# Kernel optimization log

Hardware: AMD Instinct MI355X
Metric: run time of the kernel (lower is better)

## Reference

```python
import jax, jax.numpy as jnp
import numpy as np

D_MODEL = 1024
N_HEADS = 16
HEAD_DIM = D_MODEL // N_HEADS
D_FF = 4096
EPS = 1e-5


def setup_inputs() -> dict:
    key = jax.random.key(0)
    ks = jax.random.split(key, 12)
    s = 0.02
    return {
        "x": jax.random.normal(ks[0], (2, 2048, D_MODEL), jnp.float32),
        "wq": jax.random.normal(ks[1], (D_MODEL, D_MODEL), jnp.float32) * s,
        "bq": jnp.zeros((D_MODEL,), jnp.float32),
        "wk": jax.random.normal(ks[2], (D_MODEL, D_MODEL), jnp.float32) * s,
        "bk": jnp.zeros((D_MODEL,), jnp.float32),
        "wv": jax.random.normal(ks[3], (D_MODEL, D_MODEL), jnp.float32) * s,
        "bv": jnp.zeros((D_MODEL,), jnp.float32),
        "wo": jax.random.normal(ks[4], (D_MODEL, D_MODEL), jnp.float32) * s,
        "bo": jnp.zeros((D_MODEL,), jnp.float32),
        "w1": jax.random.normal(ks[5], (D_MODEL, D_FF), jnp.float32) * s,
        "b1": jnp.zeros((D_FF,), jnp.float32),
        "w2": jax.random.normal(ks[6], (D_FF, D_MODEL), jnp.float32) * s,
        "b2": jnp.zeros((D_MODEL,), jnp.float32),
        "g1": jnp.ones((D_MODEL,), jnp.float32),
        "be1": jnp.zeros((D_MODEL,), jnp.float32),
        "g2": jnp.ones((D_MODEL,), jnp.float32),
        "be2": jnp.zeros((D_MODEL,), jnp.float32),
    }


def _layer_norm(x, g, b):
    mu = jnp.mean(x, axis=-1, keepdims=True)
    var = jnp.var(x, axis=-1, keepdims=True)
    return (x - mu) * jax.lax.rsqrt(var + EPS) * g + b


def reference(x, wq, bq, wk, bk, wv, bv, wo, bo, w1, b1, w2, b2, g1, be1, g2, be2):
    B, S, D = x.shape
    nx = _layer_norm(x, g1, be1)
    # projections -> [B, H, S, d]
    def split_heads(t):
        return t.reshape(B, S, N_HEADS, HEAD_DIM).transpose(0, 2, 1, 3)
    q = split_heads(nx @ wq + bq)
    k = split_heads(nx @ wk + bk)
    v = split_heads(nx @ wv + bv)
    scores = jnp.einsum("bhqd,bhkd->bhqk", q, k) / jnp.sqrt(jnp.float32(HEAD_DIM))
    attn = jax.nn.softmax(scores, axis=-1)
    out = jnp.einsum("bhqk,bhkd->bhqd", attn, v)
    out = out.transpose(0, 2, 1, 3).reshape(B, S, D)
    x = x + (out @ wo + bo)
    nx = _layer_norm(x, g2, be2)
    ff = jax.nn.relu(nx @ w1 + b1) @ w2 + b2
    return x + ff
```

## Files before the change

kernel.cpp:

```cpp
#include <hip/hip_runtime.h>


typedef __attribute__((ext_vector_type(8))) unsigned short u16x8;
typedef __attribute__((ext_vector_type(4))) unsigned short u16x4;
typedef __attribute__((ext_vector_type(8))) __bf16 bf16x8;
typedef __attribute__((ext_vector_type(4))) float f32x4;
typedef __attribute__((ext_vector_type(4))) unsigned int u32x4;

#define C_SCALE 0.1803368801111f

static __device__ __forceinline__ unsigned short f2b(float f) {
    return __builtin_bit_cast(unsigned short, (__bf16)f);
}
static __device__ __forceinline__ float b2f(unsigned short h) {
    unsigned u = ((unsigned)h) << 16;
    float f;
    __builtin_memcpy(&f, &u, 4);
    return f;
}

static __device__ __forceinline__ void async_cp16(
    const unsigned short* g, unsigned short* l)
{
    __builtin_amdgcn_global_load_lds(
        (const __attribute__((address_space(1))) unsigned int*)g,
        (__attribute__((address_space(3))) unsigned int*)l,
        16, 0, 0);
}

__global__ __launch_bounds__(256) void transpose_all_k(
    const float* __restrict__ wq, const float* __restrict__ wk,
    const float* __restrict__ wv, const float* __restrict__ wo,
    const float* __restrict__ w1, const float* __restrict__ w2,
    unsigned short* __restrict__ wqkvT, unsigned short* __restrict__ woT,
    unsigned short* __restrict__ w1T, unsigned short* __restrict__ w2T)
{
    __shared__ unsigned short tile[32][33];
    const int ti = blockIdx.x;
    const float* in;
    unsigned short* out;
    int R, C, bi, bj;
    float sc = 1.0f;
    if (ti < 4096) {
        R = 1024; C = 1024;
        bi = (ti & 1023) >> 5; bj = ti & 31;
        int z = ti >> 10;
        in = (z == 0) ? wq : (z == 1) ? wk : (z == 2) ? wv : wo;
        out = (z < 3) ? wqkvT + (size_t)z * 1024 * 1024 : woT;
        if (z == 1) sc = C_SCALE;
    } else if (ti < 8192) {
        R = 1024; C = 4096;
        int l = ti - 4096;
        bi = l >> 7; bj = l & 127;
        in = w1; out = w1T;
    } else {
        R = 4096; C = 1024;
        int l = ti - 8192;
        bi = l >> 5; bj = l & 31;
        in = w2; out = w2T;
    }
    const int tx = threadIdx.x & 31, ty = threadIdx.x >> 5;
#pragma unroll
    for (int rr = 0; rr < 4; ++rr) {
        int r = ty + rr * 8;
        tile[r][tx] = f2b(in[(size_t)(bi * 32 + r) * C + bj * 32 + tx] * sc);
    }
    __syncthreads();
#pragma unroll
    for (int rr = 0; rr < 4; ++rr) {
        int r = ty + rr * 8;
        out[(size_t)(bj * 32 + r) * R + bi * 32 + tx] = tile[tx][r];
    }
}

__global__ __launch_bounds__(256) void concat3_k(
    const float* __restrict__ a, const float* __restrict__ b,
    const float* __restrict__ c, float* __restrict__ o)
{
    int t = blockIdx.x * 256 + threadIdx.x;
    float v = (t < 1024) ? a[t]
            : ((t < 2048) ? b[t - 1024] * C_SCALE : c[t - 2048]);
    o[t] = v;
}

__global__ __launch_bounds__(256) void ln_kernel(
    const float* __restrict__ x, const float* __restrict__ g,
    const float* __restrict__ be, unsigned short* __restrict__ o)
{
    const int row = blockIdx.x;
    const int t = threadIdx.x;
    const float* xr = x + (size_t)row * 1024;
    float4 v4 = *reinterpret_cast<const float4*>(&xr[t * 4]);
    float f[4] = {v4.x, v4.y, v4.z, v4.w};
    float s = f[0] + f[1] + f[2] + f[3];
    float ss = f[0] * f[0] + f[1] * f[1] + f[2] * f[2] + f[3] * f[3];
#pragma unroll
    for (int d = 1; d < 64; d <<= 1) {
        s += __shfl_xor(s, d);
        ss += __shfl_xor(ss, d);
    }
    __shared__ float sb[4], ssb[4];
    const int wave = t >> 6;
    if ((t & 63) == 0) { sb[wave] = s; ssb[wave] = ss; }
    __syncthreads();
    s = sb[0] + sb[1] + sb[2] + sb[3];
    ss = ssb[0] + ssb[1] + ssb[2] + ssb[3];
    const float mu = s * (1.0f / 1024.0f);
    const float var = ss * (1.0f / 1024.0f) - mu * mu;
    const float rs = rsqrtf(var + 1e-5f);
    u16x4 r4;
#pragma unroll
    for (int j = 0; j < 4; ++j)
        r4[j] = f2b((f[j] - mu) * rs * g[t * 4 + j] + be[t * 4 + j]);
    *reinterpret_cast<u16x4*>(&o[(size_t)row * 1024 + t * 4]) = r4;
}

__global__ __launch_bounds__(256) void reduce_ln_kernel(
    const unsigned short* __restrict__ pa, const unsigned short* __restrict__ pb,
    const float* __restrict__ bias, const float* __restrict__ x,
    const float* __restrict__ g, const float* __restrict__ be,
    float* __restrict__ x2, unsigned short* __restrict__ o)
{
    const int row = blockIdx.x;
    const int t = threadIdx.x;
    const size_t base = (size_t)row * 1024 + t * 4;
    float4 x4 = *reinterpret_cast<const float4*>(&x[base]);
    float4 bb = *reinterpret_cast<const float4*>(&bias[t * 4]);
    float f[4] = {x4.x + bb.x, x4.y + bb.y, x4.z + bb.z, x4.w + bb.w};
#pragma unroll
    for (int z = 0; z < 2; ++z) {
        u16x4 va = *reinterpret_cast<const u16x4*>(&pa[(size_t)z * 4096 * 1024 + base]);
        u16x4 vb = *reinterpret_cast<const u16x4*>(&pb[(size_t)z * 4096 * 1024 + base]);
#pragma unroll
        for (int j = 0; j < 4; ++j) f[j] += b2f(va[j]) + b2f(vb[j]);
    }
    *reinterpret_cast<float4*>(&x2[base]) = {f[0], f[1], f[2], f[3]};
    float s = f[0] + f[1] + f[2] + f[3];
    float ss = f[0] * f[0] + f[1] * f[1] + f[2] * f[2] + f[3] * f[3];
#pragma unroll
    for (int d = 1; d < 64; d <<= 1) {
        s += __shfl_xor(s, d);
        ss += __shfl_xor(ss, d);
    }
    __shared__ float sb[4], ssb[4];
    const int wave = t >> 6;
    if ((t & 63) == 0) { sb[wave] = s; ssb[wave] = ss; }
    __syncthreads();
    s = sb[0] + sb[1] + sb[2] + sb[3];
    ss = ssb[0] + ssb[1] + ssb[2] + ssb[3];
    const float mu = s * (1.0f / 1024.0f);
    const float var = ss * (1.0f / 1024.0f) - mu * mu;
    const float rs = rsqrtf(var + 1e-5f);
    u16x4 r4;
#pragma unroll
    for (int j = 0; j < 4; ++j)
        r4[j] = f2b((f[j] - mu) * rs * g[t * 4 + j] + be[t * 4 + j]);
    *reinterpret_cast<u16x4*>(&o[base]) = r4;
}

__global__ __launch_bounds__(256) void reduce_out4_k(
    const unsigned short* __restrict__ pa, const unsigned short* __restrict__ pb,
    const float* __restrict__ bias, const float* __restrict__ x2,
    float* __restrict__ out)
{
    const size_t i4 = ((size_t)blockIdx.x * 256 + threadIdx.x) * 4;
    float4 x4 = *reinterpret_cast<const float4*>(&x2[i4]);
    float4 bb = *reinterpret_cast<const float4*>(&bias[i4 & 1023]);
    float a0 = x4.x + bb.x, a1 = x4.y + bb.y, a2 = x4.z + bb.z, a3 = x4.w + bb.w;
#pragma unroll
    for (int z = 0; z < 2; ++z) {
        u16x4 va = *reinterpret_cast<const u16x4*>(&pa[(size_t)z * 4096 * 1024 + i4]);
        u16x4 vb = *reinterpret_cast<const u16x4*>(&pb[(size_t)z * 4096 * 1024 + i4]);
        a0 += b2f(va[0]) + b2f(vb[0]);
        a1 += b2f(va[1]) + b2f(vb[1]);
        a2 += b2f(va[2]) + b2f(vb[2]);
        a3 += b2f(va[3]) + b2f(vb[3]);
    }
    *reinterpret_cast<float4*>(&out[i4]) = {a0, a1, a2, a3};
}

template<int MODE, int RELU>
__global__ __launch_bounds__(256, 4) void gemm_bt(
    const unsigned short* __restrict__ A, int lda,
    const unsigned short* __restrict__ Bt, int ldb,
    const float* __restrict__ bias,
    void* __restrict__ Cv, void* __restrict__ Cv2, int N, int Kloop)
{
    __shared__ unsigned short As[128 * 32];
    __shared__ unsigned short Bs[128 * 32];
    const int t = threadIdx.x;
    const int wave = t >> 6, lane = t & 63;
    const int quad = lane >> 4, l16 = lane & 15;
    const int wm = wave >> 1, wn = wave & 1;
    const int m0 = blockIdx.y * 128;
    const int n0 = blockIdx.x * 128;
    const int k0 = blockIdx.z * Kloop;
    const int rl = lane >> 2;
    const int cl = (lane & 3) * 8;

    f32x4 acc[4][4];
#pragma unroll
    for (int mi = 0; mi < 4; ++mi)
#pragma unroll
        for (int ni = 0; ni < 4; ++ni) acc[mi][ni] = {0.f, 0.f, 0.f, 0.f};

    for (int kt = 0; kt < Kloop; kt += 32) {
#pragma unroll
        for (int j = 0; j < 4; ++j) {
            int c = wave * 4 + j;
            if (c < 8) {
                async_cp16(&A[(size_t)(m0 + c * 16 + rl) * lda + k0 + kt + cl],
                           &As[c * 512 + lane * 8]);
            } else {
                int bc = c - 8;
                async_cp16(&Bt[(size_t)(n0 + bc * 16 + rl) * ldb + k0 + kt + cl],
                           &Bs[bc * 512 + lane * 8]);
            }
        }
        __syncthreads();
        bf16x8 af[4], bfr[4];
#pragma unroll
        for (int mi = 0; mi < 4; ++mi)
            af[mi] = __builtin_bit_cast(bf16x8,
                *reinterpret_cast<const u16x8*>(&As[(wm * 64 + mi * 16 + l16) * 32 + quad * 8]));
#pragma unroll
        for (int ni = 0; ni < 4; ++ni)
            bfr[ni] = __builtin_bit_cast(bf16x8,
                *reinterpret_cast<const u16x8*>(&Bs[(wn * 64 + ni * 16 + l16) * 32 + quad * 8]));
#pragma unroll
        for (int mi = 0; mi < 4; ++mi)
#pragma unroll
            for (int ni = 0; ni < 4; ++ni)
                acc[mi][ni] = __builtin_amdgcn_mfma_f32_16x16x32_bf16(
                    af[mi], bfr[ni], acc[mi][ni], 0, 0, 0);
        __syncthreads();
    }

#pragma unroll
    for (int mi = 0; mi < 4; ++mi) {
        const int gr0 = m0 + wm * 64 + mi * 16 + quad * 4;
#pragma unroll
        for (int ni = 0; ni < 4; ++ni) {
            const int gc = n0 + wn * 64 + ni * 16 + l16;
            if (MODE == 2) {
                const float bv = bias[gc];
                if (gc < 2048) {
#pragma unroll
                    for (int r = 0; r < 4; ++r)
                        ((unsigned short*)Cv)[(size_t)(gr0 + r) * 2048 + gc] =
                            f2b(acc[mi][ni][r] + bv);
                } else {
                    u16x4 pk;
#pragma unroll
                    for (int r = 0; r < 4; ++r) pk[r] = f2b(acc[mi][ni][r] + bv);
                    const int b = gr0 >> 11, s0 = gr0 & 2047;
                    *reinterpret_cast<u16x4*>(
                        &((unsigned short*)Cv2)[((size_t)b * 1024 + (gc - 2048)) * 2048 + s0]) = pk;
                }
            } else if (MODE == 5) {
                unsigned short* base = (blockIdx.z < 2)
                    ? (unsigned short*)Cv  + (size_t)blockIdx.z * 4096 * N
                    : (unsigned short*)Cv2 + (size_t)(blockIdx.z - 2) * 4096 * N;
#pragma unroll
                for (int r = 0; r < 4; ++r)
                    base[(size_t)(gr0 + r) * N + gc] = f2b(acc[mi][ni][r]);
            } else {
                const float bv = bias[gc];
#pragma unroll
                for (int r = 0; r < 4; ++r) {
                    float v = acc[mi][ni][r] + bv;
                    if (RELU) v = fmaxf(v, 0.f);
                    ((unsigned short*)Cv)[(size_t)(gr0 + r) * N + gc] = f2b(v);
                }
            }
        }
    }
}

__global__ __launch_bounds__(256, 4) void attn_kernel(
    const unsigned short* __restrict__ qkb, const unsigned short* __restrict__ vbT,
    unsigned short* __restrict__ ao)
{
    __shared__ unsigned short Ks[2][64][72];
    __shared__ unsigned short Vt[2][64][72];
    const int t = threadIdx.x;
    const int lane = t & 63;
    const int quad = lane >> 4, l16 = lane & 15;
    const int wave = t >> 6;
    const int bh = blockIdx.y;
    const int b = bh >> 4, h = bh & 15;
    const int q0 = blockIdx.x * 64 + wave * 16;
    const size_t qk_base = (size_t)b * 2048 * 2048;
    const size_t vt_base = (size_t)b * 1024 * 2048 + (size_t)h * 64 * 2048;

    bf16x8 qf[2];
#pragma unroll
    for (int kk = 0; kk < 2; ++kk)
        qf[kk] = __builtin_bit_cast(bf16x8, *reinterpret_cast<const u16x8*>(
            &qkb[qk_base + (size_t)(q0 + l16) * 2048 + h * 64 + kk * 32 + quad * 8]));

    u16x8 ones_u;
#pragma unroll
    for (int j = 0; j < 8; ++j) ones_u[j] = 0x3F80;
    const bf16x8 onesf = __builtin_bit_cast(bf16x8, ones_u);

    f32x4 o_acc[4], l_frag;
    l_frag = {0.f, 0.f, 0.f, 0.f};
#pragma unroll
    for (int nf = 0; nf < 4; ++nf) o_acc[nf] = {0.f, 0.f, 0.f, 0.f};

    const int srow0 = t >> 3, sc8 = (t & 7) * 8;
    const int srow1 = srow0 + 32;

    const unsigned short* kg0 = &qkb[qk_base + (size_t)srow0 * 2048 + 1024 + h * 64 + sc8];
    const unsigned short* kg1 = kg0 + (size_t)32 * 2048;
    const unsigned short* vg0 = &vbT[vt_base + (size_t)srow0 * 2048 + sc8];
    const unsigned short* vg1 = vg0 + (size_t)32 * 2048;

    u16x8 kr[2], vr[2];
    kr[0] = *reinterpret_cast<const u16x8*>(kg0);
    kr[1] = *reinterpret_cast<const u16x8*>(kg1);
    vr[0] = *reinterpret_cast<const u16x8*>(vg0);
    vr[1] = *reinterpret_cast<const u16x8*>(vg1);
    *reinterpret_cast<u16x8*>(&Ks[0][srow0][sc8]) = kr[0];
    *reinterpret_cast<u16x8*>(&Ks[0][srow1][sc8]) = kr[1];
    *reinterpret_cast<u16x8*>(&Vt[0][srow0][sc8]) = vr[0];
    *reinterpret_cast<u16x8*>(&Vt[0][srow1][sc8]) = vr[1];
    kr[0] = *reinterpret_cast<const u16x8*>(kg0 + (size_t)64 * 2048);
    kr[1] = *reinterpret_cast<const u16x8*>(kg1 + (size_t)64 * 2048);
    vr[0] = *reinterpret_cast<const u16x8*>(vg0 + 64);
    vr[1] = *reinterpret_cast<const u16x8*>(vg1 + 64);
    __syncthreads();

    for (int it = 0; it < 32; ++it) {
        const int cur = it & 1, nxt = cur ^ 1;
        if (it + 1 < 32) {
            *reinterpret_cast<u16x8*>(&Ks[nxt][srow0][sc8]) = kr[0];
            *reinterpret_cast<u16x8*>(&Ks[nxt][srow1][sc8]) = kr[1];
            *reinterpret_cast<u16x8*>(&Vt[nxt][srow0][sc8]) = vr[0];
            *reinterpret_cast<u16x8*>(&Vt[nxt][srow1][sc8]) = vr[1];
        }
        if (it + 2 < 32) {
            const size_t ko = (size_t)(it + 2) * 64 * 2048;
            const int vo = (it + 2) * 64;
            kr[0] = *reinterpret_cast<const u16x8*>(kg0 + ko);
            kr[1] = *reinterpret_cast<const u16x8*>(kg1 + ko);
            vr[0] = *reinterpret_cast<const u16x8*>(vg0 + vo);
            vr[1] = *reinterpret_cast<const u16x8*>(vg1 + vo);
        }

#pragma unroll
        for (int kh = 0; kh < 2; ++kh) {
            unsigned d0[2], d1[2];
#pragma unroll
            for (int kfi = 0; kfi < 2; ++kfi) {
                const int kf = kh * 2 + kfi;
                bf16x8 kfr0 = __builtin_bit_cast(bf16x8,
                    *reinterpret_cast<const u16x8*>(&Ks[cur][kf * 16 + l16][quad * 8]));
                bf16x8 kfr1 = __builtin_bit_cast(bf16x8,
                    *reinterpret_cast<const u16x8*>(&Ks[cur][kf * 16 + l16][32 + quad * 8]));
                f32x4 s = {0.f, 0.f, 0.f, 0.f};
                s = __builtin_amdgcn_mfma_f32_16x16x32_bf16(kfr0, qf[0], s, 0, 0, 0);
                s = __builtin_amdgcn_mfma_f32_16x16x32_bf16(kfr1, qf[1], s, 0, 0, 0);
                d0[kfi] = (unsigned)f2b(exp2f(s[0])) |
                          ((unsigned)f2b(exp2f(s[1])) << 16);
                d1[kfi] = (unsigned)f2b(exp2f(s[2])) |
                          ((unsigned)f2b(exp2f(s[3])) << 16);
            }
            unsigned x0 = d0[0], y0 = d0[1];
            unsigned x1 = d1[0], y1 = d1[1];
            asm("v_permlane32_swap_b32 %0, %1\n\t"
                "v_permlane16_swap_b32 %0, %1"
                : "+v"(x0), "+v"(y0));
            asm("v_permlane32_swap_b32 %0, %1\n\t"
                "v_permlane16_swap_b32 %0, %1"
                : "+v"(x1), "+v"(y1));
            u32x4 pw = {x0, x1, y0, y1};
            bf16x8 pfr = __builtin_bit_cast(bf16x8, pw);
            l_frag = __builtin_amdgcn_mfma_f32_16x16x32_bf16(
                pfr, onesf, l_frag, 0, 0, 0);
            __builtin_amdgcn_s_setprio(1);
#pragma unroll
            for (int nf = 0; nf < 4; ++nf) {
                bf16x8 vfr = __builtin_bit_cast(bf16x8,
                    *reinterpret_cast<const u16x8*>(&Vt[cur][nf * 16 + l16][kh * 32 + quad * 8]));
                o_acc[nf] = __builtin_amdgcn_mfma_f32_16x16x32_bf16(
                    pfr, vfr, o_acc[nf], 0, 0, 0);
            }
            __builtin_amdgcn_s_setprio(0);
        }
        __syncthreads();
    }

#pragma unroll
    for (int r = 0; r < 4; ++r) {
        const float inv = 1.0f / l_frag[r];
        const int row = q0 + quad * 4 + r;
#pragma unroll
        for (int nf = 0; nf < 4; ++nf)
            ao[(size_t)b * 2048 * 1024 + (size_t)row * 1024 + h * 64 + nf * 16 + l16] =
                f2b(o_acc[nf][r] * inv);
    }
}

extern "C" void kernel_launch(void* const* d_in, const int* in_sizes, int n_in,
                              void* d_out, int out_size, void* d_ws, size_t ws_size,
                              hipStream_t stream)
{
    const float* x   = (const float*)d_in[0];
    const float* wq  = (const float*)d_in[1];
    const float* bq  = (const float*)d_in[2];
    const float* wk  = (const float*)d_in[3];
    const float* bk  = (const float*)d_in[4];
    const float* wv  = (const float*)d_in[5];
    const float* bv  = (const float*)d_in[6];
    const float* wo  = (const float*)d_in[7];
    const float* bo  = (const float*)d_in[8];
    const float* w1  = (const float*)d_in[9];
    const float* b1  = (const float*)d_in[10];
    const float* w2  = (const float*)d_in[11];
    const float* b2  = (const float*)d_in[12];
    const float* g1  = (const float*)d_in[13];
    const float* be1 = (const float*)d_in[14];
    const float* g2  = (const float*)d_in[15];
    const float* be2 = (const float*)d_in[16];
    float* out = (float*)d_out;
    char*  ws  = (char*)d_ws;

    const int M = 4096, D = 1024, DFF = 4096;
    const size_t MB = 1 << 20;

    unsigned short* wqkvT = (unsigned short*)(ws + 0 * MB);
    unsigned short* woT   = (unsigned short*)(ws + 6 * MB);
    unsigned short* w1T   = (unsigned short*)(ws + 8 * MB);
    unsigned short* w2T   = (unsigned short*)(ws + 16 * MB);
    unsigned short* ln    = (unsigned short*)(ws + 24 * MB);
    unsigned short* qkb   = (unsigned short*)(ws + 32 * MB);
    unsigned short* vbT   = (unsigned short*)(ws + 48 * MB);
    unsigned short* ao    = (unsigned short*)(ws + 56 * MB);
    unsigned short* ff1   = (unsigned short*)(ws + 32 * MB);
    float*          x2    = (float*)(ws + 64 * MB);
    float*          bqkv  = (float*)(ws + 80 * MB);
    unsigned short* pHi   = (unsigned short*)(ws + 80 * MB);
    unsigned short* pOlo  = (unsigned short*)(ws + 32 * MB);
    unsigned short* pFlo  = (unsigned short*)(ws + 0 * MB);

    transpose_all_k<<<12288, 256, 0, stream>>>(wq, wk, wv, wo, w1, w2,
                                               wqkvT, woT, w1T, w2T);
    concat3_k<<<12, 256, 0, stream>>>(bq, bk, bv, bqkv);
    ln_kernel<<<M, 256, 0, stream>>>(x, g1, be1, ln);
    gemm_bt<2, 0><<<dim3(24, 32), 256, 0, stream>>>(
        ln, D, wqkvT, D, bqkv, qkb, vbT, 3072, D);
    attn_kernel<<<dim3(32, 32), 256, 0, stream>>>(qkb, vbT, ao);
    gemm_bt<5, 0><<<dim3(8, 32, 4), 256, 0, stream>>>(
        ao, D, woT, D, nullptr, pHi, pOlo, 1024, 256);
    reduce_ln_kernel<<<M, 256, 0, stream>>>(pHi, pOlo, bo, x, g2, be2, x2, ln);
    gemm_bt<0, 1><<<dim3(32, 32), 256, 0, stream>>>(
        ln, D, w1T, D, b1, ff1, nullptr, DFF, D);
    gemm_bt<5, 0><<<dim3(8, 32, 4), 256, 0, stream>>>(
        ff1, DFF, w2T, DFF, nullptr, pHi, pFlo, 1024, 1024);
    reduce_out4_k<<<4096, 256, 0, stream>>>(pHi, pFlo, b2, x2, out);
}
```

Before: 378.9 us.

## Add 256x256-tile triple-buffered GEMM kernel for QKV, FF1 and FF2

Adds a new 512-thread GEMM with 256x256 output tiles, a three-stage LDS ring fed by async global-to-LDS copies, XOR-swizzled LDS layout and MFMA issue priority raised with s_setprio. It replaces the 128x128 kernel for the QKV projection, FF1 and the split-K FF2 GEMM, aiming for more data reuse per tile and better overlap of loads with compute. The cost is far fewer blocks per launch (192 or 256), one block per CU, and higher register pressure, which can leave CUs idle on a 256-CU part.

New measurement: 358.4 us. 5.4% less time.

```diff
diff --git a/kernel.cpp b/kernel.cpp
--- a/kernel.cpp
+++ b/kernel.cpp
@@ -180,6 +180,149 @@
 }
 
 template<int MODE, int RELU>
+__global__ __launch_bounds__(512, 1) void gemm256(
+    const unsigned short* __restrict__ A, int lda,
+    const unsigned short* __restrict__ Bt, int ldb,
+    const float* __restrict__ bias,
+    void* __restrict__ Cv, void* __restrict__ Cv2, int N, int Kloop)
+{
+    __shared__ unsigned short lds[3 * 16384];
+    const int t = threadIdx.x;
+    const int wave = t >> 6, lane = t & 63;
+    const int quad = lane >> 4, l16 = lane & 15;
+    const int wm = wave >> 2, wn = wave & 3;
+    const int m0 = blockIdx.y * 256;
+    const int n0 = blockIdx.x * 256;
+    const int k0 = blockIdx.z * Kloop;
+    const int NT = Kloop >> 5;
+
+    const int sc_row = t >> 2;
+    const int sc_cb  = (t & 3) ^ ((t >> 3) & 3);
+    const unsigned short* Asrc = &A[(size_t)(m0 + sc_row) * lda + k0 + sc_cb * 8];
+    const unsigned short* Bsrc = &Bt[(size_t)(n0 + sc_row) * ldb + k0 + sc_cb * 8];
+    const size_t Astep = (size_t)128 * lda;
+    const size_t Bstep = (size_t)128 * ldb;
+    unsigned short* dstA = &lds[t * 8];
+    unsigned short* dstB = &lds[8192 + t * 8];
+
+    const int cb = quad ^ ((l16 >> 1) & 3);
+    const int aoff = (wm * 128 + l16) * 32 + cb * 8;
+    const int boff = 8192 + (wn * 64 + l16) * 32 + cb * 8;
+
+    f32x4 acc[8][4];
+#pragma unroll
+    for (int mi = 0; mi < 8; ++mi)
+#pragma unroll
+        for (int ni = 0; ni < 4; ++ni) acc[mi][ni] = {0.f, 0.f, 0.f, 0.f};
+
+    async_cp16(Asrc, dstA);
+    async_cp16(Asrc + Astep, dstA + 4096);
+    async_cp16(Bsrc, dstB);
+    async_cp16(Bsrc + Bstep, dstB + 4096);
+    if (NT > 1) {
+        async_cp16(Asrc + 32, dstA + 16384);
+        async_cp16(Asrc + Astep + 32, dstA + 16384 + 4096);
+        async_cp16(Bsrc + 32, dstB + 16384);
+        async_cp16(Bsrc + Bstep + 32, dstB + 16384 + 4096);
+        asm volatile("s_waitcnt vmcnt(4)\n\ts_barrier" ::: "memory");
+    } else {
+        asm volatile("s_waitcnt vmcnt(0)\n\ts_barrier" ::: "memory");
+    }
+
+    for (int tt = 0; tt < NT; ++tt) {
+        const int b = tt - (tt / 3) * 3;
+        const unsigned short* Lb = &lds[b * 16384];
+        const int pf = tt + 2;
+        const int bp = (pf < NT) ? (pf - (pf / 3) * 3) * 16384 : 0;
+        bf16x8 af[8], bfr[4];
+        if (pf < NT) {
+            async_cp16(Asrc + (size_t)pf * 32, &lds[bp] + t * 8);
+            async_cp16(Asrc + Astep + (size_t)pf * 32, &lds[bp] + t * 8 + 4096);
+        }
+#pragma unroll
+        for (int mi = 0; mi < 8; ++mi)
+            af[mi] = __builtin_bit_cast(bf16x8,
+                *reinterpret_cast<const u16x8*>(&Lb[aoff + mi * 512]));
+        bfr[0] = __builtin_bit_cast(bf16x8,
+            *reinterpret_cast<const u16x8*>(&Lb[boff]));
+        bfr[1] = __builtin_bit_cast(bf16x8,
+            *reinterpret_cast<const u16x8*>(&Lb[boff + 512]));
+        __builtin_amdgcn_s_setprio(1);
+#pragma unroll
+        for (int mi = 0; mi < 8; ++mi) {
+            acc[mi][0] = __builtin_amdgcn_mfma_f32_16x16x32_bf16(
+                af[mi], bfr[0], acc[mi][0], 0, 0, 0);
+            acc[mi][1] = __builtin_amdgcn_mfma_f32_16x16x32_bf16(
+                af[mi], bfr[1], acc[mi][1], 0, 0, 0);
+        }
+        __builtin_amdgcn_s_setprio(0);
+        if (pf < NT) {
+            async_cp16(Bsrc + (size_t)pf * 32, &lds[bp + 8192] + t * 8);
+            async_cp16(Bsrc + Bstep + (size_t)pf * 32, &lds[bp + 8192] + t * 8 + 4096);
+        }
+        bfr[2] = __builtin_bit_cast(bf16x8,
+            *reinterpret_cast<const u16x8*>(&Lb[boff + 1024]));
+        bfr[3] = __builtin_bit_cast(bf16x8,
+            *reinterpret_cast<const u16x8*>(&Lb[boff + 1536]));
+        __builtin_amdgcn_s_setprio(1);
+#pragma unroll
+        for (int mi = 0; mi < 8; ++mi) {
+            acc[mi][2] = __builtin_amdgcn_mfma_f32_16x16x32_bf16(
+                af[mi], bfr[2], acc[mi][2], 0, 0, 0);
+            acc[mi][3] = __builtin_amdgcn_mfma_f32_16x16x32_bf16(
+                af[mi], bfr[3], acc[mi][3], 0, 0, 0);
+        }
+        __builtin_amdgcn_s_setprio(0);
+        if (tt + 1 < NT) {
+            if (pf < NT)
+                asm volatile("s_waitcnt vmcnt(4)\n\ts_barrier" ::: "memory");
+            else
+                asm volatile("s_waitcnt vmcnt(0)\n\ts_barrier" ::: "memory");
+        }
+    }
+
+#pragma unroll
+    for (int mi = 0; mi < 8; ++mi) {
+        const int gr0 = m0 + wm * 128 + mi * 16 + quad * 4;
+#pragma unroll
+        for (int ni = 0; ni < 4; ++ni) {
+            const int gc = n0 + wn * 64 + ni * 16 + l16;
+            if (MODE == 2) {
+                const float bv = bias[gc];
+                if (gc < 2048) {
+#pragma unroll
+                    for (int r = 0; r < 4; ++r)
+                        ((unsigned short*)Cv)[(size_t)(gr0 + r) * 2048 + gc] =
+                            f2b(acc[mi][ni][r] + bv);
+                } else {
+                    u16x4 pk;
+#pragma unroll
+                    for (int r = 0; r < 4; ++r) pk[r] = f2b(acc[mi][ni][r] + bv);
+                    const int bb = gr0 >> 11, s0 = gr0 & 2047;
+                    *reinterpret_cast<u16x4*>(
+                        &((unsigned short*)Cv2)[((size_t)bb * 1024 + (gc - 2048)) * 2048 + s0]) = pk;
+                }
+            } else if (MODE == 5) {
+                unsigned short* base = (blockIdx.z < 2)
+                    ? (unsigned short*)Cv  + (size_t)blockIdx.z * 4096 * N
+                    : (unsigned short*)Cv2 + (size_t)(blockIdx.z - 2) * 4096 * N;
+#pragma unroll
+                for (int r = 0; r < 4; ++r)
+                    base[(size_t)(gr0 + r) * N + gc] = f2b(acc[mi][ni][r]);
+            } else {
+                const float bv = bias[gc];
+#pragma unroll
+                for (int r = 0; r < 4; ++r) {
+                    float v = acc[mi][ni][r] + bv;
+                    if (RELU) v = fmaxf(v, 0.f);
+                    ((unsigned short*)Cv)[(size_t)(gr0 + r) * N + gc] = f2b(v);
+                }
+            }
+        }
+    }
+}
+
+template<int MODE, int RELU>
 __global__ __launch_bounds__(256, 4) void gemm_bt(
     const unsigned short* __restrict__ A, int lda,
     const unsigned short* __restrict__ Bt, int ldb,
@@ -242,22 +385,7 @@
 #pragma unroll
         for (int ni = 0; ni < 4; ++ni) {
             const int gc = n0 + wn * 64 + ni * 16 + l16;
-            if (MODE == 2) {
-                const float bv = bias[gc];
-                if (gc < 2048) {
-#pragma unroll
-                    for (int r = 0; r < 4; ++r)
-                        ((unsigned short*)Cv)[(size_t)(gr0 + r) * 2048 + gc] =
-                            f2b(acc[mi][ni][r] + bv);
-                } else {
-                    u16x4 pk;
-#pragma unroll
-                    for (int r = 0; r < 4; ++r) pk[r] = f2b(acc[mi][ni][r] + bv);
-                    const int b = gr0 >> 11, s0 = gr0 & 2047;
-                    *reinterpret_cast<u16x4*>(
-                        &((unsigned short*)Cv2)[((size_t)b * 1024 + (gc - 2048)) * 2048 + s0]) = pk;
-                }
-            } else if (MODE == 5) {
+            if (MODE == 5) {
                 unsigned short* base = (blockIdx.z < 2)
                     ? (unsigned short*)Cv  + (size_t)blockIdx.z * 4096 * N
                     : (unsigned short*)Cv2 + (size_t)(blockIdx.z - 2) * 4096 * N;
@@ -449,15 +577,15 @@
                                                wqkvT, woT, w1T, w2T);
     concat3_k<<<12, 256, 0, stream>>>(bq, bk, bv, bqkv);
     ln_kernel<<<M, 256, 0, stream>>>(x, g1, be1, ln);
-    gemm_bt<2, 0><<<dim3(24, 32), 256, 0, stream>>>(
+    gemm256<2, 0><<<dim3(12, 16), 512, 0, stream>>>(
         ln, D, wqkvT, D, bqkv, qkb, vbT, 3072, D);
     attn_kernel<<<dim3(32, 32), 256, 0, stream>>>(qkb, vbT, ao);
     gemm_bt<5, 0><<<dim3(8, 32, 4), 256, 0, stream>>>(
         ao, D, woT, D, nullptr, pHi, pOlo, 1024, 256);
     reduce_ln_kernel<<<M, 256, 0, stream>>>(pHi, pOlo, bo, x, g2, be2, x2, ln);
-    gemm_bt<0, 1><<<dim3(32, 32), 256, 0, stream>>>(
+    gemm256<0, 1><<<dim3(16, 16), 512, 0, stream>>>(
         ln, D, w1T, D, b1, ff1, nullptr, DFF, D);
-    gemm_bt<5, 0><<<dim3(8, 32, 4), 256, 0, stream>>>(
+    gemm256<5, 0><<<dim3(4, 16, 4), 512, 0, stream>>>(
         ff1, DFF, w2T, DFF, nullptr, pHi, pFlo, 1024, 1024);
     reduce_out4_k<<<4096, 256, 0, stream>>>(pHi, pFlo, b2, x2, out);
 }
```
